# Optimization experiments

Measured on AMD Instinct MI355X. Metric: run time of the kernel, lower is better.

The kernel has to match this reference:

```python
import jax, jax.numpy as jnp
from jax import lax
import numpy as np

B, L, I, H, W, O = 256, 1024, 16, 128, 512, 4


def _linear_init(key, fan_in, fan_out):
    # mimic torch nn.Linear default: U(-1/sqrt(fan_in), 1/sqrt(fan_in))
    kw, kb = jax.random.split(key)
    lim = 1.0 / np.sqrt(fan_in)
    Wm = jax.random.uniform(kw, (fan_in, fan_out), jnp.float32, -lim, lim)
    b = jax.random.uniform(kb, (fan_out,), jnp.float32, -lim, lim)
    return Wm, b


def setup_inputs() -> dict:
    key = jax.random.key(0)
    ks = jax.random.split(key, 10)
    # strictly increasing time grid: cumsum of small positive steps
    dts = jax.random.uniform(ks[0], (B, L), jnp.float32, 0.001, 0.01)
    ts = jnp.cumsum(dts, axis=1)
    x = jax.random.normal(ks[1], (B, L, I), jnp.float32)
    Wi1, bi1 = _linear_init(ks[2], I, W)
    Wi2, bi2 = _linear_init(ks[3], W, H)
    Wf1, bf1 = _linear_init(ks[4], H, W)
    Wf2, bf2 = _linear_init(ks[5], W, W)
    Wf3, bf3 = _linear_init(ks[6], W, H * I)
    Wo1, bo1 = _linear_init(ks[7], H, 32)
    Wo2, bo2 = _linear_init(ks[8], 32, O)
    return {"ts": ts, "x": x,
            "Wi1": Wi1, "bi1": bi1, "Wi2": Wi2, "bi2": bi2,
            "Wf1": Wf1, "bf1": bf1, "Wf2": Wf2, "bf2": bf2,
            "Wf3": Wf3, "bf3": bf3,
            "Wo1": Wo1, "bo1": bo1, "Wo2": Wo2, "bo2": bo2}


def reference(ts, x, Wi1, bi1, Wi2, bi2, Wf1, bf1, Wf2, bf2, Wf3, bf3, Wo1, bo1, Wo2, bo2):
    Bq, Lq, Iq = x.shape
    Hq = Wi2.shape[1]
    # initial network: y0 = Linear(tanh(Linear(x0)))
    y0 = jnp.tanh(x[:, 0, :] @ Wi1 + bi1) @ Wi2 + bi2  # (B, H)
    # precompute per-step increments as scan inputs
    dts = (ts[:, 1:] - ts[:, :-1]).T                      # (L-1, B)
    dxs = jnp.transpose(x[:, 1:, :] - x[:, :-1, :], (1, 0, 2))  # (L-1, B, I)

    def step(y, inp):
        dt, dx = inp  # (B,), (B, I)
        h = jnp.tanh(y @ Wf1 + bf1)
        h = jnp.tanh(h @ Wf2 + bf2)
        f = (h @ Wf3 + bf3).reshape(Bq, Hq, Iq)  # vector field (B, H, I)
        dy = jnp.einsum('bij,bj->bi', f, dx)
        return y + dy * dt[:, None], None

    yT, _ = lax.scan(step, y0, (dts, dxs))
    # output head with sigmoid
    out = jax.nn.sigmoid(jnp.tanh(yT @ Wo1 + bo1) @ Wo2 + bo2)  # (B, O)
    return out
```

## Files before the change

kernel.cpp:

```cpp
#include <hip/hip_runtime.h>


constexpr int LQ = 1024, IQ = 16, HQ = 128, WQ = 512, OQ = 4;
constexpr int THREADS = 512;
constexpr size_t CSTRIDE = 49152;

typedef __attribute__((ext_vector_type(8))) short bf16x8;
typedef __attribute__((ext_vector_type(4))) float f32x4;
typedef unsigned int u32t;
typedef unsigned long long u64t;

#define MFMA16(a, b, c) __builtin_amdgcn_mfma_f32_16x16x32_bf16((a), (b), (c), 0, 0, 0)

__device__ __forceinline__ unsigned short f2bf(float f) {
  unsigned u = __builtin_bit_cast(unsigned, f);
  u += 0x7FFFu + ((u >> 16) & 1u);
  return (unsigned short)(u >> 16);
}
__device__ __forceinline__ float bf2f(unsigned short h) {
  unsigned u = ((unsigned)h) << 16;
  return __builtin_bit_cast(float, u);
}
__device__ __forceinline__ float fast_tanh(float x) {
  float e = __expf(2.0f * x);
  return 1.0f - 2.0f / (e + 1.0f);
}

__device__ __forceinline__ bf16x8 load_bfrag(const float* W, int N, int k0, int n0, int lane) {
  const int col = n0 + (lane & 15);
  const int kb  = k0 + 8 * (lane >> 4);
  bf16x8 v;
#pragma unroll
  for (int j = 0; j < 8; ++j) v[j] = (short)f2bf(W[(kb + j) * N + col]);
  return v;
}

__device__ __forceinline__ void st32a(u32t* p, u32t v) {
  __hip_atomic_store(p, v, __ATOMIC_RELAXED, __HIP_MEMORY_SCOPE_AGENT);
}
__device__ __forceinline__ u32t ld32a(const u32t* p) {
  return __hip_atomic_load(p, __ATOMIC_RELAXED, __HIP_MEMORY_SCOPE_AGENT);
}
__device__ __forceinline__ void st64a(u64t* p, u64t v) {
  __hip_atomic_store(p, v, __ATOMIC_RELAXED, __HIP_MEMORY_SCOPE_AGENT);
}
__device__ __forceinline__ u64t ld64a(const u64t* p) {
  return __hip_atomic_load(p, __ATOMIC_RELAXED, __HIP_MEMORY_SCOPE_AGENT);
}
__device__ __forceinline__ void pollf(const u32t* p, u32t want) {
  while (ld32a(p) != want) __builtin_amdgcn_s_sleep(2);
  asm volatile("" ::: "memory");
}
__device__ __forceinline__ void drain_all() { __builtin_amdgcn_s_waitcnt(0); }

constexpr int OFF_YS  = 0;
constexpr int OFF_H12 = 4352;
constexpr int OFF_RED = 20992;
constexpr int OFF_B1  = 37888;
constexpr int OFF_B2  = 39936;
constexpr int OFF_B3  = 40064;
constexpr int OFF_DX  = 40576;
constexpr int OFF_DT  = 41856;
constexpr int OFF_YP  = 41920;
constexpr int POOLSZ  = 42176;

__global__ __launch_bounds__(THREADS, 2) void cde_kernel(
    const float* __restrict__ ts,  const float* __restrict__ x,
    const float* __restrict__ Wi1, const float* __restrict__ bi1,
    const float* __restrict__ Wi2, const float* __restrict__ bi2,
    const float* __restrict__ Wf1, const float* __restrict__ bfv1,
    const float* __restrict__ Wf2, const float* __restrict__ bfv2,
    const float* __restrict__ Wf3, const float* __restrict__ bfv3,
    const float* __restrict__ Wo1, const float* __restrict__ bo1,
    const float* __restrict__ Wo2, const float* __restrict__ bo2,
    float* __restrict__ out, unsigned char* __restrict__ ws) {
  const int tid  = threadIdx.x;
  const int wave = tid >> 6;
  const int lane = tid & 63;
  const int bid  = blockIdx.x;
  const int c    = bid >> 4;
  const int r    = bid & 15;

  unsigned char* cb = ws + (size_t)c * CSTRIDE;
  u32t* fy = (u32t*)cb;
  u32t* fh = (u32t*)(cb + 256);
  unsigned short* ybuf  = (unsigned short*)(cb + 512);
  unsigned short* h2buf = (unsigned short*)(cb + 8704);

  __shared__ __align__(16) unsigned char pool[POOLSZ];
  auto y_s = (unsigned short(*)[136])(pool + OFF_YS);
  auto h1s = (unsigned short(*)[520])(pool + OFF_H12);
  auto h2s = (unsigned short(*)[520])(pool + OFF_H12);
  auto red = (float(*)[16][33])(pool + OFF_RED);
  auto h0f = (float(*)[512])(pool);
  float* b1s = (float*)(pool + OFF_B1);
  float* b2s = (float*)(pool + OFF_B2);
  float* b3s = (float*)(pool + OFF_B3);
  float* dxs = (float*)(pool + OFF_DX);
  float* y0f = (float*)(pool + OFF_DX);
  float* dtl = (float*)(pool + OFF_DT);
  unsigned short* ypack = (unsigned short*)(pool + OFF_YP);

  bf16x8 w1f[4][4];
#pragma unroll
  for (int n = 0; n < 4; ++n)
#pragma unroll
    for (int k4 = 0; k4 < 4; ++k4)
      w1f[n][k4] = load_bfrag(Wf1, WQ, 32 * k4, 64 * wave + 16 * n, lane);
  const int w_nt = wave & 1, w_q = wave >> 1;
  bf16x8 w2f[4];
#pragma unroll
  for (int kk = 0; kk < 4; ++kk)
    w2f[kk] = load_bfrag(Wf2, WQ, 32 * (4 * w_q + kk), 32 * r + 16 * w_nt, lane);
  bf16x8 w3f[16];
#pragma unroll
  for (int kt = 0; kt < 16; ++kt)
    w3f[kt] = load_bfrag(Wf3, HQ * IQ, 32 * kt, 128 * r + 16 * wave, lane);

  b1s[tid] = bi1[tid];
  if (tid < 32) b2s[tid] = bfv2[32 * r + tid];
  if (tid >= 64 && tid < 192) b3s[tid - 64] = bfv3[128 * r + (tid - 64)];

  {
    int row = tid >> 5, col0 = (tid & 31) * 16;
    const float* xr = x + ((16 * c + row) * LQ) * IQ;
    float xv[16];
#pragma unroll
    for (int j = 0; j < 16; ++j) xv[j] = xr[j];
    for (int cc = 0; cc < 16; ++cc) {
      int col = col0 + cc;
      float s = bi1[col];
#pragma unroll
      for (int j = 0; j < 16; ++j) s += xv[j] * Wi1[j * WQ + col];
      h0f[row][col] = tanhf(s);
    }
  }
  __syncthreads();
  if (tid < 128) {
    int m = tid >> 3, hl = tid & 7, hh = 8 * r + hl;
    float s = bi2[hh];
#pragma unroll 8
    for (int k = 0; k < WQ; ++k) s += h0f[m][k] * Wi2[k * HQ + hh];
    ypack[m * 8 + hl] = f2bf(s);
    y0f[m * 8 + hl] = s;
  }
  __syncthreads();
  f32x4 y4;
  {
    const int q4 = 4 * (lane >> 4);
#pragma unroll
    for (int i = 0; i < 4; ++i) y4[i] = y0f[(q4 + i) * 8 + wave];
  }
  if (tid < 32) {
    int m = tid >> 1, hf = tid & 1;
    u64t v = *(const u64t*)&ypack[m * 8 + 4 * hf];
    st64a((u64t*)(ybuf + m * HQ + 8 * r + 4 * hf), v);
  }
  drain_all();
  __syncthreads();
  if (tid == 0) st32a(fy + 0 * 32 + r, 1u);

  const int g_row = tid >> 5, g_pr = (tid & 31) >> 1;
  const int g_c4 = (tid & 31) * 4, g_c16 = (tid & 31) * 16;

  for (int t = 0; t < LQ - 1; ++t) {
    const int par = t & 1, pn = par ^ 1;
    if (tid < 256) {
      int m = tid >> 4, j = tid & 15;
      const float* xp = x + ((16 * c + m) * LQ + t) * IQ + j;
      dxs[m * 20 + j] = xp[IQ] - xp[0];
    }
    if (tid < 16) {
      const float* tp = ts + (16 * c + tid) * LQ + t;
      dtl[tid] = tp[1] - tp[0];
    }
    pollf(fy + par * 32 + g_pr, (u32t)(t + 1));
    {
      u64t v = ld64a((const u64t*)(ybuf + par * 2048 + g_row * HQ + g_c4));
      *(u64t*)&y_s[g_row][g_c4] = v;
    }
    __syncthreads();
    {
      bf16x8 af[4];
#pragma unroll
      for (int k4 = 0; k4 < 4; ++k4)
        af[k4] = *(const bf16x8*)&y_s[lane & 15][32 * k4 + 8 * (lane >> 4)];
#pragma unroll
      for (int n = 0; n < 4; ++n) {
        f32x4 acc = {0.f, 0.f, 0.f, 0.f};
#pragma unroll
        for (int k4 = 0; k4 < 4; ++k4) acc = MFMA16(af[k4], w1f[n][k4], acc);
        const int col = 64 * wave + 16 * n + (lane & 15);
        const float bb = b1s[col];
#pragma unroll
        for (int i = 0; i < 4; ++i)
          h1s[4 * (lane >> 4) + i][col] = f2bf(fast_tanh(acc[i] + bb));
      }
    }
    __syncthreads();
    {
      f32x4 a0 = {0.f, 0.f, 0.f, 0.f}, a1 = {0.f, 0.f, 0.f, 0.f};
#pragma unroll
      for (int kk = 0; kk < 2; ++kk) {
        const bf16x8 f0 = *(const bf16x8*)&h1s[lane & 15][32 * (4 * w_q + kk) + 8 * (lane >> 4)];
        const bf16x8 f1 = *(const bf16x8*)&h1s[lane & 15][32 * (4 * w_q + kk + 2) + 8 * (lane >> 4)];
        a0 = MFMA16(f0, w2f[kk], a0);
        a1 = MFMA16(f1, w2f[kk + 2], a1);
      }
#pragma unroll
      for (int i = 0; i < 4; ++i)
        red[wave][4 * (lane >> 4) + i][lane & 15] = a0[i] + a1[i];
    }
    __syncthreads();
    if (tid < 256) {
      int row = tid >> 4, cp = tid & 15;
      int c0 = 2 * cp, c1 = c0 + 1, nt = cp >> 3, l0 = c0 & 15, l1 = c1 & 15;
      float v0 = b2s[c0], v1 = b2s[c1];
#pragma unroll
      for (int q = 0; q < 4; ++q) {
        v0 += red[(q << 1) | nt][row][l0];
        v1 += red[(q << 1) | nt][row][l1];
      }
      u32t pk = (u32t)f2bf(fast_tanh(v0)) | ((u32t)f2bf(fast_tanh(v1)) << 16);
      st32a((u32t*)(h2buf + par * 8192 + row * WQ + 32 * r + c0), pk);
    }
    drain_all();
    __syncthreads();
    if (tid == 0) st32a(fh + par * 32 + r, (u32t)(t + 1));
    pollf(fh + par * 32 + g_pr, (u32t)(t + 1));
    {
      const u64t* p = (const u64t*)(h2buf + par * 8192 + g_row * WQ + g_c16);
      u64t v0 = ld64a(p), v1 = ld64a(p + 1), v2 = ld64a(p + 2), v3 = ld64a(p + 3);
      u64t* d = (u64t*)&h2s[g_row][g_c16];
      d[0] = v0; d[1] = v1; d[2] = v2; d[3] = v3;
    }
    __syncthreads();
    {
      f32x4 ac0 = {0.f, 0.f, 0.f, 0.f}, ac1 = {0.f, 0.f, 0.f, 0.f};
      f32x4 ac2 = {0.f, 0.f, 0.f, 0.f}, ac3 = {0.f, 0.f, 0.f, 0.f};
#pragma unroll
      for (int kt = 0; kt < 16; kt += 4) {
        const bf16x8 a0 = *(const bf16x8*)&h2s[lane & 15][32 * kt + 8 * (lane >> 4)];
        const bf16x8 a1 = *(const bf16x8*)&h2s[lane & 15][32 * (kt + 1) + 8 * (lane >> 4)];
        const bf16x8 a2 = *(const bf16x8*)&h2s[lane & 15][32 * (kt + 2) + 8 * (lane >> 4)];
        const bf16x8 a3 = *(const bf16x8*)&h2s[lane & 15][32 * (kt + 3) + 8 * (lane >> 4)];
        ac0 = MFMA16(a0, w3f[kt], ac0);
        ac1 = MFMA16(a1, w3f[kt + 1], ac1);
        ac2 = MFMA16(a2, w3f[kt + 2], ac2);
        ac3 = MFMA16(a3, w3f[kt + 3], ac3);
      }
      const float bb = b3s[16 * wave + (lane & 15)];
      const int q4 = 4 * (lane >> 4);
      f32x4 p;
#pragma unroll
      for (int i = 0; i < 4; ++i)
        p[i] = (ac0[i] + ac1[i] + ac2[i] + ac3[i] + bb) * dxs[(q4 + i) * 20 + (lane & 15)];
#pragma unroll
      for (int m = 1; m <= 8; m <<= 1) {
#pragma unroll
        for (int i = 0; i < 4; ++i) p[i] += __shfl_xor(p[i], m, 64);
      }
#pragma unroll
      for (int i = 0; i < 4; ++i) y4[i] += p[i] * dtl[q4 + i];
      if ((lane & 15) == 0) {
#pragma unroll
        for (int i = 0; i < 4; ++i) ypack[(q4 + i) * 8 + wave] = f2bf(y4[i]);
      }
    }
    __syncthreads();
    if (tid < 32) {
      int m = tid >> 1, hf = tid & 1;
      u64t v = *(const u64t*)&ypack[m * 8 + 4 * hf];
      st64a((u64t*)(ybuf + pn * 2048 + m * HQ + 8 * r + 4 * hf), v);
    }
    drain_all();
    __syncthreads();
    if (tid == 0) st32a(fy + pn * 32 + r, (u32t)(t + 2));
  }

  if (r == 0) {
    pollf(fy + 1 * 32 + g_pr, (u32t)LQ);
    {
      u64t v = ld64a((const u64t*)(ybuf + 2048 + g_row * HQ + g_c4));
      *(u64t*)&y_s[g_row][g_c4] = v;
    }
    __syncthreads();
    float* gep = (float*)(pool + OFF_RED);
    {
      int m = tid >> 5, o = tid & 31;
      float s = bo1[o];
#pragma unroll 8
      for (int k = 0; k < HQ; ++k) s += bf2f(y_s[m][k]) * Wo1[k * 32 + o];
      gep[m * 32 + o] = tanhf(s);
    }
    __syncthreads();
    if (tid < 64) {
      int m = tid >> 2, oo = tid & 3;
      float s = bo2[oo];
#pragma unroll
      for (int k = 0; k < 32; ++k) s += gep[m * 32 + k] * Wo2[k * OQ + oo];
      out[(16 * c + m) * OQ + oo] = 1.f / (1.f + __expf(-s));
    }
  }
}

extern "C" void kernel_launch(void* const* d_in, const int* in_sizes, int n_in,
                              void* d_out, int out_size, void* d_ws, size_t ws_size,
                              hipStream_t stream) {
  (void)in_sizes; (void)n_in; (void)out_size; (void)ws_size;
  hipMemsetAsync(d_ws, 0, 16 * CSTRIDE, stream);
  cde_kernel<<<dim3(256), dim3(THREADS), 0, stream>>>(
      (const float*)d_in[0],  (const float*)d_in[1],
      (const float*)d_in[2],  (const float*)d_in[3],
      (const float*)d_in[4],  (const float*)d_in[5],
      (const float*)d_in[6],  (const float*)d_in[7],
      (const float*)d_in[8],  (const float*)d_in[9],
      (const float*)d_in[10], (const float*)d_in[11],
      (const float*)d_in[12], (const float*)d_in[13],
      (const float*)d_in[14], (const float*)d_in[15],
      (float*)d_out, (unsigned char*)d_ws);
}
```

Before: 7.121 ms.

## Fold dx into Wf3 contraction and reduce dy via global atomics

Reorders the vector-field contraction so each block multiplies its local slice of h2 (scaled by dx) against a K-split of Wf3. The bias term is folded in through an extra MFMA on block r==0. Partial dy sums are accumulated across the 16 cooperating blocks with float atomic adds into a 4-deep ring buffer, guarded by a counter barrier. This removes the second cross-block h2 exchange and barrier per step and keeps y in fp32 registers. In exchange it adds atomic traffic and a different rounding path, since h*dx is rounded to bf16 and atomics reduce in nondeterministic order.

```diff
diff --git a/kernel.cpp b/kernel.cpp
--- a/kernel.cpp
+++ b/kernel.cpp
@@ -25,6 +25,11 @@
   float e = __expf(2.0f * x);
   return 1.0f - 2.0f / (e + 1.0f);
 }
+__device__ __forceinline__ u32t cvtpk(float lo, float hi) {
+  u32t r;
+  asm("v_cvt_pk_bf16_f32 %0, %1, %2" : "=v"(r) : "v"(lo), "v"(hi));
+  return r;
+}
 
 __device__ __forceinline__ bf16x8 load_bfrag(const float* W, int N, int k0, int n0, int lane) {
   const int col = n0 + (lane & 15);
@@ -47,22 +52,25 @@
 __device__ __forceinline__ u64t ld64a(const u64t* p) {
   return __hip_atomic_load(p, __ATOMIC_RELAXED, __HIP_MEMORY_SCOPE_AGENT);
 }
-__device__ __forceinline__ void pollf(const u32t* p, u32t want) {
-  while (ld32a(p) != want) __builtin_amdgcn_s_sleep(2);
+__device__ __forceinline__ void faddA(float* p, float v) {
+  __hip_atomic_fetch_add(p, v, __ATOMIC_RELAXED, __HIP_MEMORY_SCOPE_AGENT);
+}
+__device__ __forceinline__ void pollge(const u32t* p, u32t want) {
+  while (ld32a(p) < want) __builtin_amdgcn_s_sleep(2);
   asm volatile("" ::: "memory");
 }
 __device__ __forceinline__ void drain_all() { __builtin_amdgcn_s_waitcnt(0); }
 
 constexpr int OFF_YS  = 0;
-constexpr int OFF_H12 = 4352;
+constexpr int OFF_H1  = 4352;
 constexpr int OFF_RED = 20992;
 constexpr int OFF_B1  = 37888;
 constexpr int OFF_B2  = 39936;
-constexpr int OFF_B3  = 40064;
-constexpr int OFF_DX  = 40576;
-constexpr int OFF_DT  = 41856;
-constexpr int OFF_YP  = 41920;
-constexpr int POOLSZ  = 42176;
+constexpr int OFF_H2S = 40064;
+constexpr int OFF_DX  = 41344;
+constexpr int OFF_DT  = 42624;
+constexpr int POOLSZ  = 42688;
+
 
 __global__ __launch_bounds__(THREADS, 2) void cde_kernel(
     const float* __restrict__ ts,  const float* __restrict__ x,
@@ -82,24 +90,20 @@
   const int r    = bid & 15;
 
   unsigned char* cb = ws + (size_t)c * CSTRIDE;
-  u32t* fy = (u32t*)cb;
-  u32t* fh = (u32t*)(cb + 256);
-  unsigned short* ybuf  = (unsigned short*)(cb + 512);
-  unsigned short* h2buf = (unsigned short*)(cb + 8704);
+  float* dyb  = (float*)(cb + 512);
+  float* y0b  = (float*)(cb + 33280);
+  u32t*  fy   = (u32t*)(cb + 41472);
 
   __shared__ __align__(16) unsigned char pool[POOLSZ];
   auto y_s = (unsigned short(*)[136])(pool + OFF_YS);
-  auto h1s = (unsigned short(*)[520])(pool + OFF_H12);
-  auto h2s = (unsigned short(*)[520])(pool + OFF_H12);
+  auto h1s = (unsigned short(*)[520])(pool + OFF_H1);
   auto red = (float(*)[16][33])(pool + OFF_RED);
+  auto h2s = (unsigned short(*)[40])(pool + OFF_H2S);
   auto h0f = (float(*)[512])(pool);
   float* b1s = (float*)(pool + OFF_B1);
   float* b2s = (float*)(pool + OFF_B2);
-  float* b3s = (float*)(pool + OFF_B3);
   float* dxs = (float*)(pool + OFF_DX);
-  float* y0f = (float*)(pool + OFF_DX);
   float* dtl = (float*)(pool + OFF_DT);
-  unsigned short* ypack = (unsigned short*)(pool + OFF_YP);
 
   bf16x8 w1f[4][4];
 #pragma unroll
@@ -113,13 +117,34 @@
   for (int kk = 0; kk < 4; ++kk)
     w2f[kk] = load_bfrag(Wf2, WQ, 32 * (4 * w_q + kk), 32 * r + 16 * w_nt, lane);
   bf16x8 w3f[16];
-#pragma unroll
-  for (int kt = 0; kt < 16; ++kt)
-    w3f[kt] = load_bfrag(Wf3, HQ * IQ, 32 * kt, 128 * r + 16 * wave, lane);
+  {
+    const int h = 16 * wave + (lane & 15);
+#pragma unroll
+    for (int kk = 0; kk < 16; ++kk) {
+      bf16x8 v;
+#pragma unroll
+      for (int jj = 0; jj < 8; ++jj) {
+        int Kp = 32 * kk + 8 * (lane >> 4) + jj;
+        int k = Kp >> 4, j = Kp & 15;
+        v[jj] = (short)f2bf(Wf3[(32 * r + k) * (HQ * IQ) + 16 * h + j]);
+      }
+      w3f[kk] = v;
+    }
+  }
+  bf16x8 w3b;
+  {
+    const int h = 16 * wave + (lane & 15);
+    bf16x8 v;
+#pragma unroll
+    for (int jj = 0; jj < 8; ++jj) {
+      int Kpp = 8 * (lane >> 4) + jj;
+      v[jj] = (Kpp < 16) ? (short)f2bf(bfv3[16 * h + Kpp]) : (short)0;
+    }
+    w3b = v;
+  }
 
   b1s[tid] = bi1[tid];
   if (tid < 32) b2s[tid] = bfv2[32 * r + tid];
-  if (tid >= 64 && tid < 192) b3s[tid - 64] = bfv3[128 * r + (tid - 64)];
 
   {
     int row = tid >> 5, col0 = (tid & 31) * 16;
@@ -137,49 +162,48 @@
   }
   __syncthreads();
   if (tid < 128) {
-    int m = tid >> 3, hl = tid & 7, hh = 8 * r + hl;
-    float s = bi2[hh];
+    int m = tid >> 3, hl = tid & 7;
+    float s = bi2[8 * r + hl];
 #pragma unroll 8
-    for (int k = 0; k < WQ; ++k) s += h0f[m][k] * Wi2[k * HQ + hh];
-    ypack[m * 8 + hl] = f2bf(s);
-    y0f[m * 8 + hl] = s;
-  }
+    for (int k = 0; k < WQ; ++k) s += h0f[m][k] * Wi2[k * HQ + 8 * r + hl];
+    st32a((u32t*)&y0b[m * HQ + 8 * r + hl], __builtin_bit_cast(u32t, s));
+  }
+  drain_all();
   __syncthreads();
+  if (tid == 0) st32a(fy + r, 1u);
   f32x4 y4;
   {
-    const int q4 = 4 * (lane >> 4);
-#pragma unroll
-    for (int i = 0; i < 4; ++i) y4[i] = y0f[(q4 + i) * 8 + wave];
-  }
-  if (tid < 32) {
-    int m = tid >> 1, hf = tid & 1;
-    u64t v = *(const u64t*)&ypack[m * 8 + 4 * hf];
-    st64a((u64t*)(ybuf + m * HQ + 8 * r + 4 * hf), v);
-  }
-  drain_all();
+    pollge(fy + ((tid & 31) >> 1), 1u);
+    u64t a = ld64a((const u64t*)(y0b + tid * 4));
+    u64t b = ld64a((const u64t*)(y0b + tid * 4 + 2));
+    y4[0] = __builtin_bit_cast(float, (u32t)a);
+    y4[1] = __builtin_bit_cast(float, (u32t)(a >> 32));
+    y4[2] = __builtin_bit_cast(float, (u32t)b);
+    y4[3] = __builtin_bit_cast(float, (u32t)(b >> 32));
+  }
   __syncthreads();
-  if (tid == 0) st32a(fy + 0 * 32 + r, 1u);
-
-  const int g_row = tid >> 5, g_pr = (tid & 31) >> 1;
-  const int g_c4 = (tid & 31) * 4, g_c16 = (tid & 31) * 16;
+
+  const float* xrow = x + ((size_t)(16 * c + (tid >> 4))) * LQ * IQ + (tid & 15);
+  const float* tsp  = ts + (size_t)(16 * c + tid) * LQ;
 
   for (int t = 0; t < LQ - 1; ++t) {
-    const int par = t & 1, pn = par ^ 1;
-    if (tid < 256) {
-      int m = tid >> 4, j = tid & 15;
-      const float* xp = x + ((16 * c + m) * LQ + t) * IQ + j;
-      dxs[m * 20 + j] = xp[IQ] - xp[0];
-    }
-    if (tid < 16) {
-      const float* tp = ts + (16 * c + tid) * LQ + t;
-      dtl[tid] = tp[1] - tp[0];
-    }
-    pollf(fy + par * 32 + g_pr, (u32t)(t + 1));
-    {
-      u64t v = ld64a((const u64t*)(ybuf + par * 2048 + g_row * HQ + g_c4));
-      *(u64t*)&y_s[g_row][g_c4] = v;
-    }
-    __syncthreads();
+    const int A = t & 3;
+    const u32t target = 16u * (u32t)((t >> 2) + 1);
+    float* dyA = dyb + A * 2048;
+    float* dyZ = dyb + ((t + 2) & 3) * 2048;
+    u32t* cntA = (u32t*)(cb + A * 128);
+
+    if (tid < 64) st64a((u64t*)(dyZ + r * 128 + tid * 2), 0ull);
+    float xa = 0.f, xb = 0.f, ta = 0.f, tb = 0.f;
+    if (tid < 256) { const float* xp = xrow + t * IQ; xa = xp[0]; xb = xp[IQ]; }
+    if (tid < 16)  { ta = tsp[t]; tb = tsp[t + 1]; }
+    {
+      u32t w0 = cvtpk(y4[0], y4[1]), w1 = cvtpk(y4[2], y4[3]);
+      *(u64t*)&y_s[tid >> 5][4 * (tid & 31)] = ((u64t)w1 << 32) | (u64t)w0;
+    }
+    __syncthreads();
+    if (tid < 256) dxs[(tid >> 4) * 20 + (tid & 15)] = xb - xa;
+    if (tid < 16)  dtl[tid] = tb - ta;
     {
       bf16x8 af[4];
 #pragma unroll
@@ -221,76 +245,86 @@
         v0 += red[(q << 1) | nt][row][l0];
         v1 += red[(q << 1) | nt][row][l1];
       }
-      u32t pk = (u32t)f2bf(fast_tanh(v0)) | ((u32t)f2bf(fast_tanh(v1)) << 16);
-      st32a((u32t*)(h2buf + par * 8192 + row * WQ + 32 * r + c0), pk);
+      *(u32t*)&h2s[row][c0] = (u32t)f2bf(fast_tanh(v0)) | ((u32t)f2bf(fast_tanh(v1)) << 16);
+    }
+    __syncthreads();
+    {
+      const int b = lane & 15;
+      u32t rd[16];
+      {
+        const uint4* hp = (const uint4*)&h2s[b][0];
+        uint4 q0 = hp[0], q1 = hp[1], q2 = hp[2], q3 = hp[3];
+        rd[0] = q0.x; rd[1] = q0.y; rd[2]  = q0.z; rd[3]  = q0.w;
+        rd[4] = q1.x; rd[5] = q1.y; rd[6]  = q1.z; rd[7]  = q1.w;
+        rd[8] = q2.x; rd[9] = q2.y; rd[10] = q2.z; rd[11] = q2.w;
+        rd[12] = q3.x; rd[13] = q3.y; rd[14] = q3.z; rd[15] = q3.w;
+      }
+      float dxsel[8];
+#pragma unroll
+      for (int jj = 0; jj < 8; ++jj) {
+        float lo = dxs[b * 20 + jj], hi = dxs[b * 20 + 8 + jj];
+        dxsel[jj] = (lane & 16) ? hi : lo;
+      }
+      f32x4 acc = {0.f, 0.f, 0.f, 0.f};
+#pragma unroll
+      for (int kk = 0; kk < 16; ++kk) {
+        u32t d = rd[kk];
+        float ha = bf2f((unsigned short)(d & 0xffffu));
+        float hb = bf2f((unsigned short)(d >> 16));
+        float hv = (lane & 32) ? hb : ha;
+        int4 ai;
+        ai.x = (int)cvtpk(hv * dxsel[0], hv * dxsel[1]);
+        ai.y = (int)cvtpk(hv * dxsel[2], hv * dxsel[3]);
+        ai.z = (int)cvtpk(hv * dxsel[4], hv * dxsel[5]);
+        ai.w = (int)cvtpk(hv * dxsel[6], hv * dxsel[7]);
+        acc = MFMA16(__builtin_bit_cast(bf16x8, ai), w3f[kk], acc);
+      }
+      if (r == 0) {
+        int4 bi4;
+        if (lane & 32) {
+          bi4.x = bi4.y = bi4.z = bi4.w = 0;
+        } else {
+          bi4.x = (int)cvtpk(dxsel[0], dxsel[1]);
+          bi4.y = (int)cvtpk(dxsel[2], dxsel[3]);
+          bi4.z = (int)cvtpk(dxsel[4], dxsel[5]);
+          bi4.w = (int)cvtpk(dxsel[6], dxsel[7]);
+        }
+        acc = MFMA16(__builtin_bit_cast(bf16x8, bi4), w3b, acc);
+      }
+      const int g = lane >> 4, hcol = 16 * wave + b;
+#pragma unroll
+      for (int i = 0; i < 4; ++i)
+        faddA(dyA + (4 * g + i) * HQ + hcol, acc[i]);
     }
     drain_all();
     __syncthreads();
-    if (tid == 0) st32a(fh + par * 32 + r, (u32t)(t + 1));
-    pollf(fh + par * 32 + g_pr, (u32t)(t + 1));
-    {
-      const u64t* p = (const u64t*)(h2buf + par * 8192 + g_row * WQ + g_c16);
-      u64t v0 = ld64a(p), v1 = ld64a(p + 1), v2 = ld64a(p + 2), v3 = ld64a(p + 3);
-      u64t* d = (u64t*)&h2s[g_row][g_c16];
-      d[0] = v0; d[1] = v1; d[2] = v2; d[3] = v3;
-    }
-    __syncthreads();
-    {
-      f32x4 ac0 = {0.f, 0.f, 0.f, 0.f}, ac1 = {0.f, 0.f, 0.f, 0.f};
-      f32x4 ac2 = {0.f, 0.f, 0.f, 0.f}, ac3 = {0.f, 0.f, 0.f, 0.f};
-#pragma unroll
-      for (int kt = 0; kt < 16; kt += 4) {
-        const bf16x8 a0 = *(const bf16x8*)&h2s[lane & 15][32 * kt + 8 * (lane >> 4)];
-        const bf16x8 a1 = *(const bf16x8*)&h2s[lane & 15][32 * (kt + 1) + 8 * (lane >> 4)];
-        const bf16x8 a2 = *(const bf16x8*)&h2s[lane & 15][32 * (kt + 2) + 8 * (lane >> 4)];
-        const bf16x8 a3 = *(const bf16x8*)&h2s[lane & 15][32 * (kt + 3) + 8 * (lane >> 4)];
-        ac0 = MFMA16(a0, w3f[kt], ac0);
-        ac1 = MFMA16(a1, w3f[kt + 1], ac1);
-        ac2 = MFMA16(a2, w3f[kt + 2], ac2);
-        ac3 = MFMA16(a3, w3f[kt + 3], ac3);
-      }
-      const float bb = b3s[16 * wave + (lane & 15)];
-      const int q4 = 4 * (lane >> 4);
-      f32x4 p;
-#pragma unroll
-      for (int i = 0; i < 4; ++i)
-        p[i] = (ac0[i] + ac1[i] + ac2[i] + ac3[i] + bb) * dxs[(q4 + i) * 20 + (lane & 15)];
-#pragma unroll
-      for (int m = 1; m <= 8; m <<= 1) {
-#pragma unroll
-        for (int i = 0; i < 4; ++i) p[i] += __shfl_xor(p[i], m, 64);
-      }
-#pragma unroll
-      for (int i = 0; i < 4; ++i) y4[i] += p[i] * dtl[q4 + i];
-      if ((lane & 15) == 0) {
-#pragma unroll
-        for (int i = 0; i < 4; ++i) ypack[(q4 + i) * 8 + wave] = f2bf(y4[i]);
-      }
-    }
-    __syncthreads();
-    if (tid < 32) {
-      int m = tid >> 1, hf = tid & 1;
-      u64t v = *(const u64t*)&ypack[m * 8 + 4 * hf];
-      st64a((u64t*)(ybuf + pn * 2048 + m * HQ + 8 * r + 4 * hf), v);
-    }
-    drain_all();
-    __syncthreads();
-    if (tid == 0) st32a(fy + pn * 32 + r, (u32t)(t + 2));
+    if (tid == 0) __hip_atomic_fetch_add(cntA, 1u, __ATOMIC_RELAXED, __HIP_MEMORY_SCOPE_AGENT);
+    pollge(cntA, target);
+    {
+      u64t a = ld64a((const u64t*)(dyA + tid * 4));
+      u64t b = ld64a((const u64t*)(dyA + tid * 4 + 2));
+      const float dtv = dtl[tid >> 5];
+      y4[0] += __builtin_bit_cast(float, (u32t)a) * dtv;
+      y4[1] += __builtin_bit_cast(float, (u32t)(a >> 32)) * dtv;
+      y4[2] += __builtin_bit_cast(float, (u32t)b) * dtv;
+      y4[3] += __builtin_bit_cast(float, (u32t)(b >> 32)) * dtv;
+    }
   }
 
   if (r == 0) {
-    pollf(fy + 1 * 32 + g_pr, (u32t)LQ);
-    {
-      u64t v = ld64a((const u64t*)(ybuf + 2048 + g_row * HQ + g_c4));
-      *(u64t*)&y_s[g_row][g_c4] = v;
-    }
-    __syncthreads();
-    float* gep = (float*)(pool + OFF_RED);
+    float* yf = (float*)(pool + OFF_RED);
+    {
+      int m = tid >> 5, h4 = 4 * (tid & 31);
+#pragma unroll
+      for (int i = 0; i < 4; ++i) yf[m * HQ + h4 + i] = y4[i];
+    }
+    __syncthreads();
+    float* gep = (float*)(pool + OFF_YS);
     {
       int m = tid >> 5, o = tid & 31;
       float s = bo1[o];
 #pragma unroll 8
-      for (int k = 0; k < HQ; ++k) s += bf2f(y_s[m][k]) * Wo1[k * 32 + o];
+      for (int k = 0; k < HQ; ++k) s += yf[m * HQ + k] * Wo1[k * 32 + o];
       gep[m * 32 + o] = tanhf(s);
     }
     __syncthreads();
```

Measured after the change: 6.570 ms. -7.7%, faster.
